# Performance work log

Hardware: AMD Instinct MI355X
Metric: run time of the kernel (lower is better)

## Reference

```python
import jax, jax.numpy as jnp
import numpy as np

B, N, A = 8, 256, 180  # batch, resolution (even), n_angles


def setup_inputs() -> dict:
    key = jax.random.key(0)
    imgs = jax.random.normal(jax.random.fold_in(key, 0), (B, N, N), dtype=jnp.float32)
    # uniformly spaced projection angles over [0, pi)
    angles = jnp.linspace(0.0, np.pi, A, endpoint=False).astype(jnp.float32)
    return {"imgs": imgs, "angles": angles}


def _radon_forward(imgs, angles):
    """Parallel-beam Radon forward projection via bilinear ray sampling.

    imgs:   [B, N, N] float image batch
    angles: [A] float projection angles (radians)
    returns sinogram [B, A, N] (detector count == resolution, unit step along ray)
    """
    n = imgs.shape[-1]
    dtype = imgs.dtype
    c = (n - 1) / 2.0  # image center in pixel coords
    s = jnp.arange(n, dtype=dtype) - c  # detector positions, centered
    t = s                                # integration steps along each ray
    cos = jnp.cos(angles)[:, None, None]  # [A,1,1]
    sin = jnp.sin(angles)[:, None, None]
    # Sample point for (angle a, detector s_i, step t_j), in pixel coordinates.
    x = s[None, :, None] * cos - t[None, None, :] * sin + c  # [A, N, N]
    y = s[None, :, None] * sin + t[None, None, :] * cos + c  # [A, N, N]

    x0 = jnp.floor(x)
    y0 = jnp.floor(y)
    wx = x - x0
    wy = y - y0
    x0i = x0.astype(jnp.int32)
    y0i = y0.astype(jnp.int32)

    def corner(xi, yi, w):
        # zero-padding outside the image: mask out-of-range samples
        inb = (xi >= 0) & (xi < n) & (yi >= 0) & (yi < n)
        xc = jnp.clip(xi, 0, n - 1)
        yc = jnp.clip(yi, 0, n - 1)
        vals = imgs[:, yc, xc]  # gather -> [B, A, N, N]
        return vals * (w * inb.astype(dtype))[None]

    acc = (corner(x0i, y0i, (1.0 - wx) * (1.0 - wy))
           + corner(x0i + 1, y0i, wx * (1.0 - wy))
           + corner(x0i, y0i + 1, (1.0 - wx) * wy)
           + corner(x0i + 1, y0i + 1, wx * wy))
    return acc.sum(axis=-1)  # line integral along t -> [B, A, N]


def reference(imgs, angles):
    return _radon_forward(imgs, angles)
```

## Files before the change

kernel.cpp:

```cpp
#include <hip/hip_runtime.h>
#include <hip/hip_fp16.h>

#define NREZ 256
#define NB 8
#define NA 180

#define GW 258
#define GBYTES ((size_t)GW * GW * 16)

#define LW 44
#define LH 37
#define QTAB 0x24713560u
#define QPTAB 0x0224477113355660ull
#define CHUNK_T 16
#define NCHUNK (NREZ / CHUNK_T)

__device__ __forceinline__ __half2 bc_h2(unsigned int v) {
    return __builtin_bit_cast(__half2, v);
}

__device__ __forceinline__ void dma16(const uint4* g, uint4* l) {
    __builtin_amdgcn_global_load_lds(
        (const __attribute__((address_space(1))) void*)g,
        (__attribute__((address_space(3))) void*)l, 16, 0, 0);
}

__global__ __launch_bounds__(256) void build_fp16g(const float* __restrict__ img,
                                                   uint4* __restrict__ gbuf) {
    const int gy = blockIdx.x;
    for (int gx = threadIdx.x; gx < GW; gx += 256) {
        uint4 v = make_uint4(0u, 0u, 0u, 0u);
        const int x = gx - 1, y = gy - 1;
        if (x >= 0 && x < NREZ && y >= 0 && y < NREZ) {
            const int p = (y << 8) + x;
            unsigned short h[NB];
#pragma unroll
            for (int b = 0; b < NB; ++b)
                h[b] = __half_as_ushort(__float2half_rn(img[b * (NREZ * NREZ) + p]));
            v.x = (unsigned)h[0] | ((unsigned)h[1] << 16);
            v.y = (unsigned)h[2] | ((unsigned)h[3] << 16);
            v.z = (unsigned)h[4] | ((unsigned)h[5] << 16);
            v.w = (unsigned)h[6] | ((unsigned)h[7] << 16);
        }
        gbuf[(size_t)gy * GW + gx] = v;
    }
}

__global__ __launch_bounds__(256) void radon_dma(const uint4* __restrict__ gbuf,
                                                 const float* __restrict__ angles,
                                                 float* __restrict__ out) {
    __shared__ uint4 tile[LW * LH];

    const int a = blockIdx.x;
    const int tid = threadIdx.x;
    const int wave = tid >> 6;
    const int lane = tid & 63;
    const int s_sub = lane & 7;
    const int t_sub = lane >> 3;
    const int sIdx = blockIdx.y * 32 + wave * 8 + s_sub;

    const float C = 127.5f;
    float sn, cs;
    sincosf(angles[a], &sn, &cs);
    const float s = (float)sIdx - C;
    const float xs = fmaf(s, cs, C);
    const float ys = fmaf(s, sn, C);

    const float s_lo = (float)(blockIdx.y * 32) - C;
    const float s_hi = s_lo + 31.f;
    const float xsl = fmaf(s_lo, cs, C), xsh = fmaf(s_hi, cs, C);
    const float ysl = fmaf(s_lo, sn, C), ysh = fmaf(s_hi, sn, C);

    auto window = [&](int ck, int& bxs, int& bys, bool& interior) {
        const float t_lo = (float)(ck * CHUNK_T) - C;
        const float t_hi = t_lo + 15.f;
        const float x00 = fmaf(t_lo, -sn, xsl), x01 = fmaf(t_hi, -sn, xsl);
        const float x10 = fmaf(t_lo, -sn, xsh), x11 = fmaf(t_hi, -sn, xsh);
        const float y00 = fmaf(t_lo, cs, ysl), y01 = fmaf(t_hi, cs, ysl);
        const float y10 = fmaf(t_lo, cs, ysh), y11 = fmaf(t_hi, cs, ysh);
        const int bx = (int)floorf(fminf(fminf(x00, x01), fminf(x10, x11)));
        const int by = (int)floorf(fminf(fminf(y00, y01), fminf(y10, y11)));
        bxs = min(max(bx, -1), 220);
        bys = min(max(by, -1), 220);
        interior = (bx >= 0) && (by >= 0) && (bx <= 219) && (by <= 219);
    };

    auto stage = [&](int bxs, int bys) {
#pragma unroll
        for (int k = 0; k < 10; ++k) {
            const int row = wave + 4 * k;
            if (row < LH && lane < 37) {
                const unsigned qr = (QTAB >> ((row & 7) << 2)) & 7u;
                const uint4* gp = gbuf + (size_t)(bys + row + 1) * GW + (bxs + 1) + lane;
                dma16(gp, &tile[row * LW + qr]);
            }
        }
    };

    float accf[NB];
#pragma unroll
    for (int b = 0; b < NB; ++b) accf[b] = 0.f;
    const __half2 hz = __float2half2_rn(0.f);

    int bxs, bys;
    bool interior;
    window(0, bxs, bys, interior);
    stage(bxs, bys);

    for (int ck = 0; ck < NCHUNK; ++ck) {
        __syncthreads();

        const float t_lo = (float)(ck * CHUNK_T) - C;
        __half2 acc01 = hz, acc23 = hz, acc45 = hz, acc67 = hz;

        auto samp = [&](float tt, bool chk) {
            const float x = fmaf(tt, -sn, xs);
            const float y = fmaf(tt, cs, ys);
            const float xf = floorf(x), yf = floorf(y);
            const int u0 = (int)xf, v0 = (int)yf;
            if (!chk || (u0 >= -1 && u0 <= 255 && v0 >= -1 && v0 <= 255)) {
                const float wu = x - xf, wv = y - yf;
                const float au = 1.f - wu, av = 1.f - wv;
                const __half2 w00 = __float2half2_rn(au * av);
                const __half2 w10 = __float2half2_rn(wu * av);
                const __half2 w01 = __float2half2_rn(au * wv);
                const __half2 w11 = __float2half2_rn(wu * wv);
                const int dx = u0 - bxs;
                const int r = v0 - bys;
                const unsigned pp = (unsigned)(QPTAB >> ((r & 7) << 3));
                const int b00 = r * LW + (int)(pp & 7u) + dx;
                const int b10 = (r + 1) * LW + (int)((pp >> 4) & 7u) + dx;
                const uint4 p00 = tile[b00];
                const uint4 p10 = tile[b00 + 1];
                const uint4 p01 = tile[b10];
                const uint4 p11 = tile[b10 + 1];
                acc01 = __hfma2(w00, bc_h2(p00.x), acc01);
                acc01 = __hfma2(w10, bc_h2(p10.x), acc01);
                acc01 = __hfma2(w01, bc_h2(p01.x), acc01);
                acc01 = __hfma2(w11, bc_h2(p11.x), acc01);
                acc23 = __hfma2(w00, bc_h2(p00.y), acc23);
                acc23 = __hfma2(w10, bc_h2(p10.y), acc23);
                acc23 = __hfma2(w01, bc_h2(p01.y), acc23);
                acc23 = __hfma2(w11, bc_h2(p11.y), acc23);
                acc45 = __hfma2(w00, bc_h2(p00.z), acc45);
                acc45 = __hfma2(w10, bc_h2(p10.z), acc45);
                acc45 = __hfma2(w01, bc_h2(p01.z), acc45);
                acc45 = __hfma2(w11, bc_h2(p11.z), acc45);
                acc67 = __hfma2(w00, bc_h2(p00.w), acc67);
                acc67 = __hfma2(w10, bc_h2(p10.w), acc67);
                acc67 = __hfma2(w01, bc_h2(p01.w), acc67);
                acc67 = __hfma2(w11, bc_h2(p11.w), acc67);
            }
        };

        if (interior) {
            samp(t_lo + (float)t_sub, false);
            samp(t_lo + (float)(t_sub + 8), false);
        } else {
            samp(t_lo + (float)t_sub, true);
            samp(t_lo + (float)(t_sub + 8), true);
        }

        accf[0] += __low2float(acc01); accf[1] += __high2float(acc01);
        accf[2] += __low2float(acc23); accf[3] += __high2float(acc23);
        accf[4] += __low2float(acc45); accf[5] += __high2float(acc45);
        accf[6] += __low2float(acc67); accf[7] += __high2float(acc67);

        __syncthreads();

        if (ck + 1 < NCHUNK) {
            window(ck + 1, bxs, bys, interior);
            stage(bxs, bys);
        }
    }

#pragma unroll
    for (int b = 0; b < NB; ++b) {
        float v = accf[b];
        v += __shfl_xor(v, 8);
        v += __shfl_xor(v, 16);
        v += __shfl_xor(v, 32);
        accf[b] = v;
    }
    if (t_sub == 0) {
#pragma unroll
        for (int b = 0; b < NB; ++b) {
            out[(b * NA + a) * NREZ + sIdx] = accf[b];
        }
    }
}

__global__ __launch_bounds__(256) void radon_plain(const float* __restrict__ img,
                                                   const float* __restrict__ angles,
                                                   float* __restrict__ out) {
    const int a = blockIdx.x;
    const int tid = threadIdx.x;
    const int wave = tid >> 6;
    const int lane = tid & 63;
    const int s_sub = lane & 7;
    const int t_sub = lane >> 3;
    const int sIdx = blockIdx.y * 32 + wave * 8 + s_sub;
    const float c = 127.5f;
    float sn, cs;
    sincosf(angles[a], &sn, &cs);
    const float s = (float)sIdx - c;
    float acc[NB];
#pragma unroll
    for (int b = 0; b < NB; ++b) acc[b] = 0.f;
    for (int j = 0; j < NREZ / 8; ++j) {
        const float tt = (float)(t_sub + 8 * j) - c;
        const float x = s * cs - tt * sn + c;
        const float y = s * sn + tt * cs + c;
        const float xf = floorf(x), yf = floorf(y);
        const int u0 = (int)xf, v0 = (int)yf;
        if (u0 < -1 || u0 >= NREZ || v0 < -1 || v0 >= NREZ) continue;
        const float wu = x - xf, wv = y - yf;
        const bool iu0 = (u0 >= 0), iu1 = (u0 + 1 <= NREZ - 1);
        const bool iv0 = (v0 >= 0), iv1 = (v0 + 1 <= NREZ - 1);
        const float w00 = (1.f - wu) * (1.f - wv) * ((iu0 && iv0) ? 1.f : 0.f);
        const float w10 = wu * (1.f - wv) * ((iu1 && iv0) ? 1.f : 0.f);
        const float w01 = (1.f - wu) * wv * ((iu0 && iv1) ? 1.f : 0.f);
        const float w11 = wu * wv * ((iu1 && iv1) ? 1.f : 0.f);
        const int u0c = min(max(u0, 0), NREZ - 1);
        const int u1c = min(u0 + 1, NREZ - 1);
        const int v0c = min(max(v0, 0), NREZ - 1);
        const int v1c = min(v0 + 1, NREZ - 1);
#pragma unroll
        for (int b = 0; b < NB; ++b) {
            const float* p = img + b * (NREZ * NREZ);
            acc[b] += w00 * p[v0c * NREZ + u0c] + w10 * p[v0c * NREZ + u1c] +
                      w01 * p[v1c * NREZ + u0c] + w11 * p[v1c * NREZ + u1c];
        }
    }
#pragma unroll
    for (int b = 0; b < NB; ++b) {
        float v = acc[b];
        v += __shfl_xor(v, 8);
        v += __shfl_xor(v, 16);
        v += __shfl_xor(v, 32);
        acc[b] = v;
    }
    if (t_sub == 0) {
#pragma unroll
        for (int b = 0; b < NB; ++b) out[(b * NA + a) * NREZ + sIdx] = acc[b];
    }
}

extern "C" void kernel_launch(void* const* d_in, const int* in_sizes, int n_in,
                              void* d_out, int out_size, void* d_ws, size_t ws_size,
                              hipStream_t stream) {
    (void)in_sizes; (void)n_in; (void)out_size;
    const float* imgs = (const float*)d_in[0];
    const float* angles = (const float*)d_in[1];
    float* out = (float*)d_out;

    dim3 grid(NA, NREZ / 32);
    if (ws_size >= GBYTES) {
        uint4* gbuf = (uint4*)d_ws;
        build_fp16g<<<GW, 256, 0, stream>>>(imgs, gbuf);
        radon_dma<<<grid, 256, 0, stream>>>(gbuf, angles, out);
    } else {
        radon_plain<<<grid, 256, 0, stream>>>(imgs, angles, out);
    }
}
```

Before: 97.75 us.

## Use larger 32-step chunks with new lane mapping and LDS-based final reduction

Doubles the ray-step chunk to 32, enlarging the staged LDS tile to 47x47 and removing the per-row swizzle tables. Lanes are remapped so 32 consecutive detectors share a wave row, and each thread now takes four samples per chunk. The shuffle tree is replaced by a shared-memory cross-wave reduction with coalesced stores. This halves the number of barrier/stage rounds, but it drops the bank-conflict swizzle and uses more LDS per block, which can cause bank conflicts and lower occupancy.

```diff
diff --git a/kernel.cpp b/kernel.cpp
--- a/kernel.cpp
+++ b/kernel.cpp
@@ -8,11 +8,9 @@
 #define GW 258
 #define GBYTES ((size_t)GW * GW * 16)
 
-#define LW 44
-#define LH 37
-#define QTAB 0x24713560u
-#define QPTAB 0x0224477113355660ull
-#define CHUNK_T 16
+#define LW 47
+#define LH 47
+#define CHUNK_T 32
 #define NCHUNK (NREZ / CHUNK_T)
 
 __device__ __forceinline__ __half2 bc_h2(unsigned int v) {
@@ -46,18 +44,19 @@
     }
 }
 
-__global__ __launch_bounds__(256) void radon_dma(const uint4* __restrict__ gbuf,
-                                                 const float* __restrict__ angles,
-                                                 float* __restrict__ out) {
+__global__ __launch_bounds__(256, 4) void radon_dma(const uint4* __restrict__ gbuf,
+                                                    const float* __restrict__ angles,
+                                                    float* __restrict__ out) {
     __shared__ uint4 tile[LW * LH];
 
     const int a = blockIdx.x;
     const int tid = threadIdx.x;
     const int wave = tid >> 6;
     const int lane = tid & 63;
-    const int s_sub = lane & 7;
-    const int t_sub = lane >> 3;
-    const int sIdx = blockIdx.y * 32 + wave * 8 + s_sub;
+    const int ls = lane & 31;
+    const int lp = lane >> 5;
+    const int sIdx = blockIdx.y * 32 + ls;
+    const int tw = 2 * wave + lp;
 
     const float C = 127.5f;
     float sn, cs;
@@ -73,26 +72,25 @@
 
     auto window = [&](int ck, int& bxs, int& bys, bool& interior) {
         const float t_lo = (float)(ck * CHUNK_T) - C;
-        const float t_hi = t_lo + 15.f;
+        const float t_hi = t_lo + 31.f;
         const float x00 = fmaf(t_lo, -sn, xsl), x01 = fmaf(t_hi, -sn, xsl);
         const float x10 = fmaf(t_lo, -sn, xsh), x11 = fmaf(t_hi, -sn, xsh);
         const float y00 = fmaf(t_lo, cs, ysl), y01 = fmaf(t_hi, cs, ysl);
         const float y10 = fmaf(t_lo, cs, ysh), y11 = fmaf(t_hi, cs, ysh);
         const int bx = (int)floorf(fminf(fminf(x00, x01), fminf(x10, x11)));
         const int by = (int)floorf(fminf(fminf(y00, y01), fminf(y10, y11)));
-        bxs = min(max(bx, -1), 220);
-        bys = min(max(by, -1), 220);
-        interior = (bx >= 0) && (by >= 0) && (bx <= 219) && (by <= 219);
+        bxs = min(max(bx, -1), 210);
+        bys = min(max(by, -1), 210);
+        interior = (bx >= 0) && (by >= 0) && (bx <= 210) && (by <= 210);
     };
 
     auto stage = [&](int bxs, int bys) {
 #pragma unroll
-        for (int k = 0; k < 10; ++k) {
+        for (int k = 0; k < 12; ++k) {
             const int row = wave + 4 * k;
-            if (row < LH && lane < 37) {
-                const unsigned qr = (QTAB >> ((row & 7) << 2)) & 7u;
+            if (row < LH && lane < LW) {
                 const uint4* gp = gbuf + (size_t)(bys + row + 1) * GW + (bxs + 1) + lane;
-                dma16(gp, &tile[row * LW + qr]);
+                dma16(gp, &tile[row * LW]);
             }
         }
     };
@@ -127,9 +125,8 @@
                 const __half2 w11 = __float2half2_rn(wu * wv);
                 const int dx = u0 - bxs;
                 const int r = v0 - bys;
-                const unsigned pp = (unsigned)(QPTAB >> ((r & 7) << 3));
-                const int b00 = r * LW + (int)(pp & 7u) + dx;
-                const int b10 = (r + 1) * LW + (int)((pp >> 4) & 7u) + dx;
+                const int b00 = r * LW + dx;
+                const int b10 = b00 + LW;
                 const uint4 p00 = tile[b00];
                 const uint4 p10 = tile[b00 + 1];
                 const uint4 p01 = tile[b10];
@@ -154,11 +151,13 @@
         };
 
         if (interior) {
-            samp(t_lo + (float)t_sub, false);
-            samp(t_lo + (float)(t_sub + 8), false);
+#pragma unroll
+            for (int it = 0; it < 4; ++it)
+                samp(t_lo + (float)(tw + 8 * it), false);
         } else {
-            samp(t_lo + (float)t_sub, true);
-            samp(t_lo + (float)(t_sub + 8), true);
+#pragma unroll
+            for (int it = 0; it < 4; ++it)
+                samp(t_lo + (float)(tw + 8 * it), true);
         }
 
         accf[0] += __low2float(acc01); accf[1] += __high2float(acc01);
@@ -175,18 +174,21 @@
     }
 
 #pragma unroll
-    for (int b = 0; b < NB; ++b) {
-        float v = accf[b];
-        v += __shfl_xor(v, 8);
-        v += __shfl_xor(v, 16);
-        v += __shfl_xor(v, 32);
-        accf[b] = v;
-    }
-    if (t_sub == 0) {
-#pragma unroll
-        for (int b = 0; b < NB; ++b) {
-            out[(b * NA + a) * NREZ + sIdx] = accf[b];
-        }
+    for (int b = 0; b < NB; ++b) accf[b] += __shfl_xor(accf[b], 32);
+
+    float4* red4 = (float4*)tile;
+    if (lane < 32) {
+        red4[(wave * 32 + lane) * 2 + 0] = make_float4(accf[0], accf[1], accf[2], accf[3]);
+        red4[(wave * 32 + lane) * 2 + 1] = make_float4(accf[4], accf[5], accf[6], accf[7]);
+    }
+    __syncthreads();
+    {
+        const float* red = (const float*)tile;
+        const int b = tid >> 5;
+        const int ss = tid & 31;
+        const int base = ss * 8 + b;
+        const float sum = red[base] + red[256 + base] + red[512 + base] + red[768 + base];
+        out[(b * NA + a) * NREZ + blockIdx.y * 32 + ss] = sum;
     }
 }
 
```

New measurement: 90.85 us. 7.1% less time.
